# Kernel optimization log

Measured on AMD Instinct MI355X. Metric: run time of the kernel, lower is better.

Reference implementation:

```python
import jax, jax.numpy as jnp
import numpy as np

C = 0.01          # curvature
SQRT_C = C ** 0.5 # 0.1
R = 16            # number of diagonal blocks = out_features / block_size
BS = 256          # block_size
D = R * BS        # 4096


def _artanh(x):
    # Matches torch Artanh: clamp input, grad is 1/(1-xc^2) (straight-through clamp)
    xc = jnp.clip(x, -1.0 + 1e-5, 1.0 - 1e-5)
    xc = x + jax.lax.stop_gradient(xc - x)
    return 0.5 * (jnp.log(1.0 + xc) - jnp.log(1.0 - xc))


def _tanh(x, clamp=15.0):
    return jnp.tanh(jnp.clip(x, -clamp, clamp))


def _norm(x):
    return jnp.linalg.norm(x, axis=-1, keepdims=True)


def _forward(x, weights):
    # expmap0 (poincare ball)
    u_norm = jnp.maximum(_norm(x), 1e-5)
    h = _tanh(SQRT_C * u_norm) * x / (SQRT_C * u_norm)
    # fix_filt = output_hyperbolic.data  -> detach
    h = jax.lax.stop_gradient(h)

    # mobius_matvec with block-diagonal weight; equivalent batched block matmul:
    # mx = h @ block_diag(W_1..W_r).T  ==  per-block h_r @ W_r.T
    xb = h.reshape(h.shape[:-1] + (R, BS))            # [..., r, bs]
    mx = jnp.einsum('...rk,rjk->...rj', xb, weights)  # [..., r, bs]
    mx = mx.reshape(h.shape)

    x_norm = jnp.maximum(_norm(h), 1e-5)
    mx_norm = _norm(mx)
    res_c = _tanh(mx_norm / x_norm * _artanh(SQRT_C * x_norm)) * mx / (mx_norm * SQRT_C)
    cond = jnp.all(mx == 0, axis=-1, keepdims=True)
    res = jnp.where(cond, jnp.zeros((), dtype=res_c.dtype), res_c)

    # _project onto the ball
    nrm = jnp.maximum(_norm(res), 1e-5)
    maxnorm = (1.0 - 1e-3) / SQRT_C
    res = jnp.where(nrm > maxnorm, res / nrm * maxnorm, res)

    # logmap0 (poincare ball)
    y_norm = jnp.maximum(_norm(res), 1e-5)
    return res / y_norm / SQRT_C * _artanh(SQRT_C * y_norm)


def setup_inputs() -> dict:
    key = jax.random.key(0)
    k1, k2 = jax.random.split(key)
    x = jax.random.normal(k1, (4, 2048, D), dtype=jnp.float32)
    # params: init is stack of identity blocks; add small noise so math is non-trivial
    eye = jnp.broadcast_to(jnp.eye(BS, dtype=jnp.float32), (R, BS, BS))
    weights = eye + 0.02 * jax.random.normal(k2, (R, BS, BS), dtype=jnp.float32)
    return {"x": x, "weights": weights}


def reference(x, weights):
    return _forward(x, weights)
```

## Files before the change

### kernel.cpp

```cpp
#include <hip/hip_runtime.h>
#include <hip/hip_fp16.h>


typedef __attribute__((ext_vector_type(8))) short short8;
typedef __attribute__((ext_vector_type(4))) float f32x4;
typedef __attribute__((ext_vector_type(16))) float f32x16;

__device__ __forceinline__ ushort f2bf(float f) {
  uint u = __float_as_uint(f);
  return (ushort)((u + 0x7fffu + ((u >> 16) & 1u)) >> 16);
}

__device__ __forceinline__ float gamma_of(float sx, float s2) {
  const float xnorm = sqrtf(sx);
  const float un = fmaxf(xnorm, 1e-5f);
  const float a0 = 0.1f * un;
  const float th = tanhf(fminf(a0, 15.f));
  const float c = th / a0;
  const float hn = th * (xnorm / a0);
  const float xn = fmaxf(hn, 1e-5f);
  const float sp = sqrtf(s2);
  float gt = 0.f;
  if (sp > 0.f) {
    const float s = c * sp;
    const float xc = fminf(0.1f * xn, 1.f - 1e-5f);
    const float at = 0.5f * logf((1.f + xc) / (1.f - xc));
    const float t = (s / xn) * at;
    const float tn = tanhf(fminf(t, 15.f));
    const float alpha = tn / (0.1f * s);
    const float rn = tn * 10.f;
    const float nrm = fmaxf(rn, 1e-5f);
    const float proj = (nrm > 9.99f) ? (9.99f / nrm) : 1.f;
    const float yn = fmaxf(rn * proj, 1e-5f);
    const float yc = fminf(0.1f * yn, 1.f - 1e-5f);
    const float at2 = 0.5f * logf((1.f + yc) / (1.f - yc));
    gt = c * alpha * proj * (at2 / (0.1f * yn));
  }
  return gt;
}

__global__ __launch_bounds__(256) void wrepack32(const float* __restrict__ w,
                                                 ushort* __restrict__ wb3) {
  int idx = blockIdx.x * 256 + threadIdx.x;
  int lane = idx & 63;
  int nt = (idx >> 6) & 7;
  int kf = (idx >> 9) & 15;
  int b = idx >> 13;
  int n = nt * 32 + (lane & 31);
  int k0 = kf * 16 + (lane >> 5) * 8;
  const float* src = w + ((size_t)b << 16) + (size_t)n * 256 + k0;
  float4 v0 = *reinterpret_cast<const float4*>(src);
  float4 v1 = *reinterpret_cast<const float4*>(src + 4);
  uint4 p;
  p.x = (uint)f2bf(v0.x) | ((uint)f2bf(v0.y) << 16);
  p.y = (uint)f2bf(v0.z) | ((uint)f2bf(v0.w) << 16);
  p.z = (uint)f2bf(v1.x) | ((uint)f2bf(v1.y) << 16);
  p.w = (uint)f2bf(v1.z) | ((uint)f2bf(v1.w) << 16);
  reinterpret_cast<uint4*>(wb3)[idx] = p;
}

__global__ __launch_bounds__(256, 2) void k1_kernel(const float* __restrict__ x,
                                                    const ushort* __restrict__ wb3,
                                                    float* __restrict__ ssxP,
                                                    float* __restrict__ sspP,
                                                    ushort* __restrict__ mxw) {
  __shared__ __align__(16) ushort As[4][32 * 256];

  const int tid = threadIdx.x;
  const int w = tid >> 6;
  const int l = tid & 63;
  const int lo = l & 31;
  const int hi = l >> 5;
  const int b = blockIdx.x & 15;
  const int rg = blockIdx.x >> 4;
  const size_t rowbase = (size_t)rg * 128 + (size_t)w * 32;
  char* lds = reinterpret_cast<char*>(As[w]);

  const ushort* bbase = wb3 + ((size_t)b << 16);

  short8 b0[8], b1[8];
#pragma unroll
  for (int nt = 0; nt < 8; ++nt)
    b0[nt] = *reinterpret_cast<const short8*>(bbase + (size_t)nt * 512 + l * 8);

#pragma unroll
  for (int hh = 0; hh < 2; ++hh) {
    float4 va[16];
#pragma unroll
    for (int r = 0; r < 16; ++r)
      va[r] = *reinterpret_cast<const float4*>(
          x + (rowbase + hh * 16 + r) * 4096 + b * 256 + l * 4);
#pragma unroll
    for (int r = 0; r < 16; ++r) {
      const int row = hh * 16 + r;
      uint2 p;
      p.x = (uint)f2bf(va[r].x) | ((uint)f2bf(va[r].y) << 16);
      p.y = (uint)f2bf(va[r].z) | ((uint)f2bf(va[r].w) << 16);
      uint byte = ((uint)(row * 512 + l * 8)) ^ ((uint)(row & 7) << 4);
      *reinterpret_cast<uint2*>(lds + byte) = p;
    }
  }

  f32x16 acc[8];
#pragma unroll
  for (int nt = 0; nt < 8; ++nt)
#pragma unroll
    for (int r = 0; r < 16; ++r) acc[nt][r] = 0.f;

  for (int kfp = 0; kfp < 8; ++kfp) {
    const int kfe = kfp * 2;
#pragma unroll
    for (int nt = 0; nt < 8; ++nt)
      b1[nt] = *reinterpret_cast<const short8*>(
          bbase + ((size_t)(kfe + 1) * 8 + nt) * 512 + l * 8);
    {
      uint abyte = ((uint)(lo * 512 + kfe * 32 + hi * 16)) ^ ((uint)(lo & 7) << 4);
      short8 a = *reinterpret_cast<const short8*>(lds + abyte);
#pragma unroll
      for (int nt = 0; nt < 8; ++nt)
        acc[nt] = __builtin_amdgcn_mfma_f32_32x32x16_bf16(a, b0[nt], acc[nt], 0, 0, 0);
    }
    if (kfp < 7) {
#pragma unroll
      for (int nt = 0; nt < 8; ++nt)
        b0[nt] = *reinterpret_cast<const short8*>(
            bbase + ((size_t)(kfe + 2) * 8 + nt) * 512 + l * 8);
    }
    {
      uint abyte = ((uint)(lo * 512 + (kfe + 1) * 32 + hi * 16)) ^ ((uint)(lo & 7) << 4);
      short8 a = *reinterpret_cast<const short8*>(lds + abyte);
#pragma unroll
      for (int nt = 0; nt < 8; ++nt)
        acc[nt] = __builtin_amdgcn_mfma_f32_32x32x16_bf16(a, b1[nt], acc[nt], 0, 0, 0);
    }
  }

  {
    const int row = l >> 1;
    const int seg = l & 1;
    const uint sw = (uint)(row & 7) << 4;
    float ss = 0.f;
#pragma unroll
    for (int i = 0; i < 16; ++i) {
      uint byte = ((uint)(row * 512 + seg * 256 + i * 16)) ^ sw;
      short8 v = *reinterpret_cast<const short8*>(lds + byte);
#pragma unroll
      for (int j = 0; j < 8; ++j) {
        float f = __uint_as_float(((uint)(ushort)v[j]) << 16);
        ss += f * f;
      }
    }
    ss += __shfl_xor(ss, 1, 64);
    if (seg == 0) ssxP[b * 8192 + rowbase + row] = ss;
  }

  {
    float s[16];
#pragma unroll
    for (int r = 0; r < 16; ++r) s[r] = 0.f;
#pragma unroll
    for (int nt = 0; nt < 8; ++nt)
#pragma unroll
      for (int r = 0; r < 16; ++r) s[r] += acc[nt][r] * acc[nt][r];
#pragma unroll
    for (int m = 1; m < 32; m <<= 1)
#pragma unroll
      for (int r = 0; r < 16; ++r) s[r] += __shfl_xor(s[r], m, 64);
    if (lo == 0) {
#pragma unroll
      for (int r = 0; r < 16; ++r) {
        const int row = (r & 3) + 8 * (r >> 2) + 4 * hi;
        sspP[b * 8192 + rowbase + row] = s[r];
      }
    }
  }

#pragma unroll
  for (int nt = 0; nt < 8; ++nt)
#pragma unroll
    for (int r = 0; r < 16; ++r) {
      const int row = (r & 3) + 8 * (r >> 2) + 4 * hi;
      const int col = nt * 32 + lo;
      uint byte = ((uint)(row * 512 + col * 2)) ^ ((uint)(row & 7) << 4);
      *reinterpret_cast<__half*>(lds + byte) = __float2half(acc[nt][r]);
    }

#pragma unroll
  for (int i = 0; i < 16; ++i) {
    const int row = i * 2 + hi;
    uint byte = ((uint)(row * 512 + lo * 16)) ^ ((uint)(row & 7) << 4);
    short8 v = *reinterpret_cast<const short8*>(lds + byte);
    *reinterpret_cast<short8*>(mxw + ((size_t)b * 8192 + rowbase + row) * 256 + lo * 8) = v;
  }
}

__global__ __launch_bounds__(256) void gamma_kernel(const float* __restrict__ ssxP,
                                                    const float* __restrict__ sspP,
                                                    float* __restrict__ gam) {
  const int row = blockIdx.x * 256 + threadIdx.x;
  float sx = 0.f, s2 = 0.f;
#pragma unroll
  for (int bb = 0; bb < 16; ++bb) {
    sx += ssxP[bb * 8192 + row];
    s2 += sspP[bb * 8192 + row];
  }
  gam[row] = gamma_of(sx, s2);
}

__global__ __launch_bounds__(256) void k3_kernel(const ushort* __restrict__ mxw,
                                                 const float* __restrict__ gam,
                                                 float* __restrict__ out) {
  const int t0 = blockIdx.x * 256 + threadIdx.x;
#pragma unroll 4
  for (int it = 0; it < 16; ++it) {
    const int Q = t0 + it * 524288;
    const int b = Q >> 19;
    const int r = (Q >> 6) & 8191;
    const int c = (Q & 63) << 2;
    uint2 p = *reinterpret_cast<const uint2*>(mxw + ((size_t)Q << 2));
    const float gv = gam[r];
    __half2 h0 = *reinterpret_cast<__half2*>(&p.x);
    __half2 h1 = *reinterpret_cast<__half2*>(&p.y);
    float2 f0 = __half22float2(h0);
    float2 f1 = __half22float2(h1);
    float4 o;
    o.x = f0.x * gv;
    o.y = f0.y * gv;
    o.z = f1.x * gv;
    o.w = f1.y * gv;
    *reinterpret_cast<float4*>(out + (size_t)r * 4096 + b * 256 + c) = o;
  }
}

__global__ __launch_bounds__(256) void wrepack16(const float* __restrict__ w,
                                                 ushort* __restrict__ wb2) {
  int idx = blockIdx.x * blockDim.x + threadIdx.x;
  int lane = idx & 63;
  int nt = (idx >> 6) & 15;
  int kf = (idx >> 10) & 7;
  int blk = idx >> 13;
  int g = lane >> 4, q = lane & 15;
  const float* src = w + ((size_t)blk << 16) + (size_t)(nt * 16 + q) * 256 + kf * 32 + g * 8;
  float4 v0 = *reinterpret_cast<const float4*>(src);
  float4 v1 = *reinterpret_cast<const float4*>(src + 4);
  uint4 p;
  p.x = (uint)f2bf(v0.x) | ((uint)f2bf(v0.y) << 16);
  p.y = (uint)f2bf(v0.z) | ((uint)f2bf(v0.w) << 16);
  p.z = (uint)f2bf(v1.x) | ((uint)f2bf(v1.y) << 16);
  p.w = (uint)f2bf(v1.z) | ((uint)f2bf(v1.w) << 16);
  reinterpret_cast<uint4*>(wb2)[idx] = p;
}

__global__ __launch_bounds__(1024, 4) void hyp_fused(const float* __restrict__ x,
                                                     const ushort* __restrict__ wb2,
                                                     float* __restrict__ out) {
  __shared__ ushort xs[16 * 4096];
  __shared__ float ssxp[16];
  __shared__ float sspm[16][16];
  __shared__ float gamv[16];
  const int tid = threadIdx.x;
  const int w = tid >> 6;
  const int lane = tid & 63;
  const int g = lane >> 4, q = lane & 15;
  const size_t rowbase = (size_t)blockIdx.x * 16;
  {
    const float4* xr = reinterpret_cast<const float4*>(x + (rowbase + w) * 4096);
    char* xrow = reinterpret_cast<char*>(xs);
    const uint sw = (uint)(w & 7) << 4;
    float ss = 0.f;
#pragma unroll
    for (int chunk = 0; chunk < 16; ++chunk) {
      float4 v = xr[chunk * 64 + lane];
      ss += v.x * v.x + v.y * v.y + v.z * v.z + v.w * v.w;
      uint2 p;
      p.x = (uint)f2bf(v.x) | ((uint)f2bf(v.y) << 16);
      p.y = (uint)f2bf(v.z) | ((uint)f2bf(v.w) << 16);
      uint byte = ((uint)(w * 8192 + (chunk * 64 + lane) * 8)) ^ sw;
      *reinterpret_cast<uint2*>(xrow + byte) = p;
    }
#pragma unroll
    for (int m = 32; m; m >>= 1) ss += __shfl_xor(ss, m, 64);
    if (lane == 0) ssxp[w] = ss;
  }
  __syncthreads();
  f32x4 acc[16];
#pragma unroll
  for (int nt = 0; nt < 16; ++nt) acc[nt] = (f32x4){0.f, 0.f, 0.f, 0.f};
  for (int kf = 0; kf < 8; ++kf) {
    uint abyte = ((uint)(q * 8192 + w * 512 + kf * 64 + g * 16)) ^ ((uint)(q & 7) << 4);
    short8 afr = *reinterpret_cast<const short8*>(reinterpret_cast<const char*>(xs) + abyte);
    const ushort* bkf = wb2 + ((((size_t)w * 8 + kf) * 16) << 9) + (lane << 3);
#pragma unroll
    for (int nt = 0; nt < 16; ++nt) {
      short8 bfr = *reinterpret_cast<const short8*>(bkf + (nt << 9));
      acc[nt] = __builtin_amdgcn_mfma_f32_16x16x32_bf16(afr, bfr, acc[nt], 0, 0, 0);
    }
  }
  {
    float s0 = 0.f, s1 = 0.f, s2a = 0.f, s3 = 0.f;
#pragma unroll
    for (int nt = 0; nt < 16; ++nt) {
      f32x4 a = acc[nt];
      s0 += a[0] * a[0]; s1 += a[1] * a[1]; s2a += a[2] * a[2]; s3 += a[3] * a[3];
    }
#pragma unroll
    for (int m = 1; m < 16; m <<= 1) {
      s0 += __shfl_xor(s0, m, 64); s1 += __shfl_xor(s1, m, 64);
      s2a += __shfl_xor(s2a, m, 64); s3 += __shfl_xor(s3, m, 64);
    }
    if (q == 0) {
      sspm[w][g * 4 + 0] = s0; sspm[w][g * 4 + 1] = s1;
      sspm[w][g * 4 + 2] = s2a; sspm[w][g * 4 + 3] = s3;
    }
  }
  __syncthreads();
  if (tid < 16) {
    float s2 = 0.f;
#pragma unroll
    for (int ww = 0; ww < 16; ++ww) s2 += sspm[ww][tid];
    gamv[tid] = gamma_of(ssxp[tid], s2);
  }
  __syncthreads();
  float gr[4];
#pragma unroll
  for (int j = 0; j < 4; ++j) gr[j] = gamv[g * 4 + j];
  float* orow = out + rowbase * 4096 + w * 256;
#pragma unroll
  for (int nt = 0; nt < 16; ++nt) {
    const int col = nt * 16 + q;
    f32x4 a = acc[nt];
#pragma unroll
    for (int j = 0; j < 4; ++j) orow[(size_t)(g * 4 + j) * 4096 + col] = gr[j] * a[j];
  }
}

extern "C" void kernel_launch(void* const* d_in, const int* in_sizes, int n_in,
                              void* d_out, int out_size, void* d_ws, size_t ws_size,
                              hipStream_t stream) {
  const float* x = (const float*)d_in[0];
  const float* w = (const float*)d_in[1];
  float* out = (float*)d_out;

  const size_t WB = (size_t)2 << 20;
  const size_t SSX_OFF = WB;
  const size_t SSP_OFF = WB + ((size_t)512 << 10);
  const size_t GAM_OFF = WB + ((size_t)1 << 20);
  const size_t MXW_OFF = (size_t)4 << 20;
  const size_t NEED = MXW_OFF + (size_t)16 * 8192 * 256 * 2;

  if (ws_size >= NEED) {
    ushort* wb3 = (ushort*)d_ws;
    float* ssxP = (float*)((char*)d_ws + SSX_OFF);
    float* sspP = (float*)((char*)d_ws + SSP_OFF);
    float* gamv = (float*)((char*)d_ws + GAM_OFF);
    ushort* mxw = (ushort*)((char*)d_ws + MXW_OFF);
    wrepack32<<<512, 256, 0, stream>>>(w, wb3);
    k1_kernel<<<1024, 256, 0, stream>>>(x, wb3, ssxP, sspP, mxw);
    gamma_kernel<<<32, 256, 0, stream>>>(ssxP, sspP, gamv);
    k3_kernel<<<2048, 256, 0, stream>>>(mxw, gamv, out);
  } else if (ws_size >= WB) {
    ushort* wb2 = (ushort*)d_ws;
    wrepack16<<<512, 256, 0, stream>>>(w, wb2);
    hyp_fused<<<512, 1024, 0, stream>>>(x, wb2, out);
  }
}
```

Measured before the change: 135.3 us.

## Keep weight tiles in registers and loop k1 over row tiles with prefetch

k1 now assigns each workgroup one diagonal block and 256 rows. Each wave holds the bf16 fragments for 64 output columns across the full K depth in registers and loops over eight 32-row tiles, prefetching the next x tile while the MFMAs run on the current one. The x sum of squares is taken from the fp32 values with a wave reduction, and the mx partial norms are written per wave, so the gamma kernel now sums 64 partials. This is meant to reuse the weights over more rows and overlap x loads with compute, at the cost of more registers, extra barriers per tile, and the gamma buffer now sharing workspace with the repacked weights.

```diff
diff --git a/kernel.cpp b/kernel.cpp
--- a/kernel.cpp
+++ b/kernel.cpp
@@ -64,133 +64,99 @@
                                                     float* __restrict__ ssxP,
                                                     float* __restrict__ sspP,
                                                     ushort* __restrict__ mxw) {
-  __shared__ __align__(16) ushort As[4][32 * 256];
+  __shared__ __align__(16) ushort Abuf[2][32 * 256];
 
   const int tid = threadIdx.x;
   const int w = tid >> 6;
   const int l = tid & 63;
   const int lo = l & 31;
   const int hi = l >> 5;
-  const int b = blockIdx.x & 15;
-  const int rg = blockIdx.x >> 4;
-  const size_t rowbase = (size_t)rg * 128 + (size_t)w * 32;
-  char* lds = reinterpret_cast<char*>(As[w]);
-
+  const int b = blockIdx.x >> 5;
+  const int rg = blockIdx.x & 31;
+  const size_t rowbase = (size_t)rg * 256;
   const ushort* bbase = wb3 + ((size_t)b << 16);
 
-  short8 b0[8], b1[8];
-#pragma unroll
-  for (int nt = 0; nt < 8; ++nt)
-    b0[nt] = *reinterpret_cast<const short8*>(bbase + (size_t)nt * 512 + l * 8);
-
-#pragma unroll
-  for (int hh = 0; hh < 2; ++hh) {
-    float4 va[16];
-#pragma unroll
-    for (int r = 0; r < 16; ++r)
-      va[r] = *reinterpret_cast<const float4*>(
-          x + (rowbase + hh * 16 + r) * 4096 + b * 256 + l * 4);
-#pragma unroll
-    for (int r = 0; r < 16; ++r) {
-      const int row = hh * 16 + r;
+  short8 B0[16], B1[16];
+#pragma unroll
+  for (int kf = 0; kf < 16; ++kf) {
+    B0[kf] = *reinterpret_cast<const short8*>(bbase + (size_t)(kf * 8 + w * 2 + 0) * 512 + l * 8);
+    B1[kf] = *reinterpret_cast<const short8*>(bbase + (size_t)(kf * 8 + w * 2 + 1) * 512 + l * 8);
+  }
+
+  float4 va[8];
+#pragma unroll
+  for (int r = 0; r < 8; ++r)
+    va[r] = *reinterpret_cast<const float4*>(x + (rowbase + w * 8 + r) * 4096 + b * 256 + l * 4);
+
+  for (int t = 0; t < 8; ++t) {
+    char* A = reinterpret_cast<char*>(Abuf[t & 1]);
+
+#pragma unroll
+    for (int r = 0; r < 8; ++r) {
+      const float4 v = va[r];
+      const int lrow = w * 8 + r;
       uint2 p;
-      p.x = (uint)f2bf(va[r].x) | ((uint)f2bf(va[r].y) << 16);
-      p.y = (uint)f2bf(va[r].z) | ((uint)f2bf(va[r].w) << 16);
-      uint byte = ((uint)(row * 512 + l * 8)) ^ ((uint)(row & 7) << 4);
-      *reinterpret_cast<uint2*>(lds + byte) = p;
-    }
-  }
-
-  f32x16 acc[8];
-#pragma unroll
-  for (int nt = 0; nt < 8; ++nt)
-#pragma unroll
-    for (int r = 0; r < 16; ++r) acc[nt][r] = 0.f;
-
-  for (int kfp = 0; kfp < 8; ++kfp) {
-    const int kfe = kfp * 2;
-#pragma unroll
-    for (int nt = 0; nt < 8; ++nt)
-      b1[nt] = *reinterpret_cast<const short8*>(
-          bbase + ((size_t)(kfe + 1) * 8 + nt) * 512 + l * 8);
+      p.x = (uint)f2bf(v.x) | ((uint)f2bf(v.y) << 16);
+      p.y = (uint)f2bf(v.z) | ((uint)f2bf(v.w) << 16);
+      uint byte = ((uint)(lrow * 512 + l * 8)) ^ ((uint)(r & 7) << 4);
+      *reinterpret_cast<uint2*>(A + byte) = p;
+      float ss = v.x * v.x + v.y * v.y + v.z * v.z + v.w * v.w;
+#pragma unroll
+      for (int m = 32; m; m >>= 1) ss += __shfl_xor(ss, m, 64);
+      if (l == 0) ssxP[b * 8192 + rowbase + t * 32 + lrow] = ss;
+    }
+    __syncthreads();
+
+    if (t < 7) {
+#pragma unroll
+      for (int r = 0; r < 8; ++r)
+        va[r] = *reinterpret_cast<const float4*>(
+            x + (rowbase + (t + 1) * 32 + w * 8 + r) * 4096 + b * 256 + l * 4);
+    }
+
+    f32x16 a0, a1;
+#pragma unroll
+    for (int r = 0; r < 16; ++r) { a0[r] = 0.f; a1[r] = 0.f; }
+#pragma unroll
+    for (int kf = 0; kf < 16; ++kf) {
+      uint ab = ((uint)(lo * 512 + kf * 32 + hi * 16)) ^ ((uint)(lo & 7) << 4);
+      short8 af = *reinterpret_cast<const short8*>(A + ab);
+      a0 = __builtin_amdgcn_mfma_f32_32x32x16_bf16(af, B0[kf], a0, 0, 0, 0);
+      a1 = __builtin_amdgcn_mfma_f32_32x32x16_bf16(af, B1[kf], a1, 0, 0, 0);
+    }
+
     {
-      uint abyte = ((uint)(lo * 512 + kfe * 32 + hi * 16)) ^ ((uint)(lo & 7) << 4);
-      short8 a = *reinterpret_cast<const short8*>(lds + abyte);
-#pragma unroll
-      for (int nt = 0; nt < 8; ++nt)
-        acc[nt] = __builtin_amdgcn_mfma_f32_32x32x16_bf16(a, b0[nt], acc[nt], 0, 0, 0);
-    }
-    if (kfp < 7) {
-#pragma unroll
-      for (int nt = 0; nt < 8; ++nt)
-        b0[nt] = *reinterpret_cast<const short8*>(
-            bbase + ((size_t)(kfe + 2) * 8 + nt) * 512 + l * 8);
-    }
-    {
-      uint abyte = ((uint)(lo * 512 + (kfe + 1) * 32 + hi * 16)) ^ ((uint)(lo & 7) << 4);
-      short8 a = *reinterpret_cast<const short8*>(lds + abyte);
-#pragma unroll
-      for (int nt = 0; nt < 8; ++nt)
-        acc[nt] = __builtin_amdgcn_mfma_f32_32x32x16_bf16(a, b1[nt], acc[nt], 0, 0, 0);
-    }
-  }
-
-  {
-    const int row = l >> 1;
-    const int seg = l & 1;
-    const uint sw = (uint)(row & 7) << 4;
-    float ss = 0.f;
-#pragma unroll
-    for (int i = 0; i < 16; ++i) {
-      uint byte = ((uint)(row * 512 + seg * 256 + i * 16)) ^ sw;
-      short8 v = *reinterpret_cast<const short8*>(lds + byte);
-#pragma unroll
-      for (int j = 0; j < 8; ++j) {
-        float f = __uint_as_float(((uint)(ushort)v[j]) << 16);
-        ss += f * f;
+      float s[16];
+#pragma unroll
+      for (int r = 0; r < 16; ++r) s[r] = a0[r] * a0[r] + a1[r] * a1[r];
+#pragma unroll
+      for (int m = 1; m < 32; m <<= 1)
+#pragma unroll
+        for (int r = 0; r < 16; ++r) s[r] += __shfl_xor(s[r], m, 64);
+      if (lo == 0) {
+#pragma unroll
+        for (int r = 0; r < 16; ++r) {
+          const int row = (r & 3) + 8 * (r >> 2) + 4 * hi;
+          sspP[(size_t)(b * 4 + w) * 8192 + rowbase + t * 32 + row] = s[r];
+        }
       }
     }
-    ss += __shfl_xor(ss, 1, 64);
-    if (seg == 0) ssxP[b * 8192 + rowbase + row] = ss;
-  }
-
-  {
-    float s[16];
-#pragma unroll
-    for (int r = 0; r < 16; ++r) s[r] = 0.f;
-#pragma unroll
-    for (int nt = 0; nt < 8; ++nt)
-#pragma unroll
-      for (int r = 0; r < 16; ++r) s[r] += acc[nt][r] * acc[nt][r];
-#pragma unroll
-    for (int m = 1; m < 32; m <<= 1)
-#pragma unroll
-      for (int r = 0; r < 16; ++r) s[r] += __shfl_xor(s[r], m, 64);
-    if (lo == 0) {
-#pragma unroll
-      for (int r = 0; r < 16; ++r) {
-        const int row = (r & 3) + 8 * (r >> 2) + 4 * hi;
-        sspP[b * 8192 + rowbase + row] = s[r];
-      }
-    }
-  }
-
-#pragma unroll
-  for (int nt = 0; nt < 8; ++nt)
+    __syncthreads();
+
 #pragma unroll
     for (int r = 0; r < 16; ++r) {
       const int row = (r & 3) + 8 * (r >> 2) + 4 * hi;
-      const int col = nt * 32 + lo;
-      uint byte = ((uint)(row * 512 + col * 2)) ^ ((uint)(row & 7) << 4);
-      *reinterpret_cast<__half*>(lds + byte) = __float2half(acc[nt][r]);
-    }
-
-#pragma unroll
-  for (int i = 0; i < 16; ++i) {
-    const int row = i * 2 + hi;
-    uint byte = ((uint)(row * 512 + lo * 16)) ^ ((uint)(row & 7) << 4);
-    short8 v = *reinterpret_cast<const short8*>(lds + byte);
-    *reinterpret_cast<short8*>(mxw + ((size_t)b * 8192 + rowbase + row) * 256 + lo * 8) = v;
+      *reinterpret_cast<__half*>(A + row * 512 + (w * 64 + lo) * 2) = __float2half(a0[r]);
+      *reinterpret_cast<__half*>(A + row * 512 + (w * 64 + 32 + lo) * 2) = __float2half(a1[r]);
+    }
+    __syncthreads();
+
+#pragma unroll
+    for (int r = 0; r < 8; ++r) {
+      const int lrow = w * 8 + r;
+      uint2 v = *reinterpret_cast<const uint2*>(A + lrow * 512 + l * 8);
+      *reinterpret_cast<uint2*>(mxw + ((size_t)b * 8192 + rowbase + t * 32 + lrow) * 256 + l * 4) = v;
+    }
   }
 }
 
@@ -200,10 +166,9 @@
   const int row = blockIdx.x * 256 + threadIdx.x;
   float sx = 0.f, s2 = 0.f;
 #pragma unroll
-  for (int bb = 0; bb < 16; ++bb) {
-    sx += ssxP[bb * 8192 + row];
-    s2 += sspP[bb * 8192 + row];
-  }
+  for (int bb = 0; bb < 16; ++bb) sx += ssxP[bb * 8192 + row];
+#pragma unroll
+  for (int p = 0; p < 64; ++p) s2 += sspP[(size_t)p * 8192 + row];
   gam[row] = gamma_of(sx, s2);
 }
 
@@ -344,8 +309,8 @@
   const size_t WB = (size_t)2 << 20;
   const size_t SSX_OFF = WB;
   const size_t SSP_OFF = WB + ((size_t)512 << 10);
-  const size_t GAM_OFF = WB + ((size_t)1 << 20);
-  const size_t MXW_OFF = (size_t)4 << 20;
+  const size_t MXW_OFF = SSP_OFF + ((size_t)2 << 20);
+  const size_t GAM_OFF = 0;
   const size_t NEED = MXW_OFF + (size_t)16 * 8192 * 256 * 2;
 
   if (ws_size >= NEED) {
@@ -355,7 +320,7 @@
     float* gamv = (float*)((char*)d_ws + GAM_OFF);
     ushort* mxw = (ushort*)((char*)d_ws + MXW_OFF);
     wrepack32<<<512, 256, 0, stream>>>(w, wb3);
-    k1_kernel<<<1024, 256, 0, stream>>>(x, wb3, ssxP, sspP, mxw);
+    k1_kernel<<<512, 256, 0, stream>>>(x, wb3, ssxP, sspP, mxw);
     gamma_kernel<<<32, 256, 0, stream>>>(ssxP, sspP, gamv);
     k3_kernel<<<2048, 256, 0, stream>>>(mxw, gamv, out);
   } else if (ws_size >= WB) {
```

Measured after the change: 145.4 us. 7.4% more time.
